# Kernel tuning notes

Hardware: AMD Instinct MI355X
Metric: run time of the kernel (lower is better)

The kernel has to match this reference:

```python
import jax, jax.numpy as jnp
import numpy as np

N_NODES = 100000
N_EDGES = 1600000
D = 128
H = 128


def setup_inputs() -> dict:
    key = jax.random.key(0)
    ks = jax.random.split(key, 8)
    x = jax.random.normal(ks[0], (N_NODES, D), dtype=jnp.float32)
    edge_index = jax.random.randint(ks[1], (2, N_EDGES), 0, N_NODES, dtype=jnp.int64)
    s = 1.0 / np.sqrt(D)
    Wl1 = jax.random.normal(ks[2], (H, D), dtype=jnp.float32) * s
    Wr1 = jax.random.normal(ks[3], (H, D), dtype=jnp.float32) * s
    b1 = jnp.zeros((H,), dtype=jnp.float32)
    sh = 1.0 / np.sqrt(H)
    Wl2 = jax.random.normal(ks[4], (H, H), dtype=jnp.float32) * sh
    Wr2 = jax.random.normal(ks[5], (H, H), dtype=jnp.float32) * sh
    b2 = jnp.zeros((H,), dtype=jnp.float32)
    return {"x": x, "edge_index": edge_index, "Wl1": Wl1, "Wr1": Wr1, "b1": b1,
            "Wl2": Wl2, "Wr2": Wr2, "b2": b2}


def reference(x, edge_index, Wl1, Wr1, b1, Wl2, Wr2, b2):
    N = x.shape[0]
    src, dst = edge_index[0], edge_index[1]
    # in-degree counts (shared across both layers)
    cnt = jax.ops.segment_sum(jnp.ones(src.shape, x.dtype), dst, num_segments=N)
    inv_cnt = (1.0 / jnp.maximum(cnt, 1.0))[:, None]  # [N,1], empty nbr -> 0 mean

    def sage(h, Wl, Wr, b):
        # mean aggregation of source features at destination nodes
        agg = jax.ops.segment_sum(h[src], dst, num_segments=N) * inv_cnt  # [N,F]
        return agg @ Wl.T + h @ Wr.T + b

    h = jax.nn.relu(sage(x, Wl1, Wr1, b1))
    return sage(h, Wl2, Wr2, b2)
```

## Files before the change

### kernel.cpp

```cpp
#include <hip/hip_runtime.h>
#include <hip/hip_bf16.h>

#define NN 100000
#define NE 1600000
#define BNODES 196
#define NB 511
#define NBLKA 256
#define CHUNK 6250

typedef unsigned short u16;
typedef unsigned int u32;
typedef unsigned char u8;
using frag  = __attribute__((ext_vector_type(8))) short;
using f32x4 = __attribute__((ext_vector_type(4))) float;
using v2f   = __attribute__((ext_vector_type(2))) float;

#define OFF_CNT   (0)
#define OFF_OFFS  (512u << 10)
#define OFF_BB    (1u << 20)
#define OFF_BSUM  ((1u << 20) + 4096)
#define OFF_H     (1310720u)
#define OFF_CSR   (2u << 20)
#define OFF_WT1   (8704u << 10)
#define OFF_WT2   ((8704u << 10) + 65536u)
#define OFF_HB    (9437184u)
#define OFF_H8    (35037184u)
#define OFF_REC   (47837184u)

__device__ __forceinline__ u16 f2bf(float f) {
    u32 u = __float_as_uint(f);
    u32 r = u + 0x7fffu + ((u >> 16) & 1u);
    return (u16)(r >> 16);
}

__device__ __forceinline__ bool edges_are_i64(const void* edges) {
    const long long* e = (const long long*)edges;
    bool ok = true;
#pragma unroll
    for (int i = 0; i < 4; i++) {
        long long v = e[i];
        if (v < 0 || v >= NN) ok = false;
    }
    return ok;
}

__device__ __forceinline__ u32 pk_fp8x4(float f0, float f1, float f2, float f3) {
    int r = __builtin_amdgcn_cvt_pk_fp8_f32(f0, f1, 0, false);
    r = __builtin_amdgcn_cvt_pk_fp8_f32(f2, f3, r, true);
    return (u32)r;
}

__global__ __launch_bounds__(256) void hist_kernel(const void* edges, int* H,
                                                   const float* x, u16* xb, u8* x8,
                                                   const float* Wl1, const float* Wr1,
                                                   const float* Wl2, const float* Wr2,
                                                   u16* Wst1, u16* Wst2) {
    __shared__ int h[512];
    int tid = threadIdx.x, blk = blockIdx.x;
    for (int i = tid; i < 512; i += 256) h[i] = 0;
    __syncthreads();

    {
        int gid = blk * 256 + tid;
        int idx = gid & 32767;
        const float* Wl = (gid < 32768) ? Wl1 : Wl2;
        const float* Wr = (gid < 32768) ? Wr1 : Wr2;
        u16* Wst = (gid < 32768) ? Wst1 : Wst2;
        int kb = idx >> 10, col = (idx >> 3) & 127, i = idx & 7;
        int k = kb * 8 + i;
        float v = (k < 128) ? Wl[col * 128 + k] : Wr[col * 128 + (k - 128)];
        Wst[idx] = f2bf(v);
    }
    {
        int u0 = blk * 6250;
        for (int u = u0 + tid; u < u0 + 6250; u += 256) {
            size_t base = (size_t)u * 8;
            float4 v0 = *(const float4*)(x + base);
            float4 v1 = *(const float4*)(x + base + 4);
            uint4 w;
            w.x = (u32)f2bf(v0.x) | ((u32)f2bf(v0.y) << 16);
            w.y = (u32)f2bf(v0.z) | ((u32)f2bf(v0.w) << 16);
            w.z = (u32)f2bf(v1.x) | ((u32)f2bf(v1.y) << 16);
            w.w = (u32)f2bf(v1.z) | ((u32)f2bf(v1.w) << 16);
            *(uint4*)(xb + base) = w;
            uint2 q;
            q.x = pk_fp8x4(v0.x, v0.y, v0.z, v0.w);
            q.y = pk_fp8x4(v1.x, v1.y, v1.z, v1.w);
            *(uint2*)(x8 + base) = q;
        }
    }
    bool f = edges_are_i64(edges);
    int lo = blk * CHUNK, hi = lo + CHUNK;
    if (f) {
        const long long* dst = (const long long*)edges + NE;
        for (int i = lo + tid; i < hi; i += 256)
            atomicAdd(&h[(int)__builtin_nontemporal_load(&dst[i]) / BNODES], 1);
    } else {
        const int* dst = (const int*)edges + NE;
        for (int i = lo + tid; i < hi; i += 256)
            atomicAdd(&h[__builtin_nontemporal_load(&dst[i]) / BNODES], 1);
    }
    __syncthreads();
    for (int i = tid; i < 512; i += 256) H[blk * 512 + i] = h[i];
}

__global__ __launch_bounds__(256) void scan1_kernel(int* H, int* bsum) {
    int tid = threadIdx.x;
    int lane = tid & 63;
    int b = blockIdx.x * 4 + (tid >> 6);
    int v0 = H[(lane * 4 + 0) * 512 + b];
    int v1 = H[(lane * 4 + 1) * 512 + b];
    int v2 = H[(lane * 4 + 2) * 512 + b];
    int v3 = H[(lane * 4 + 3) * 512 + b];
    int t = v0 + v1 + v2 + v3;
    int sc = t;
#pragma unroll
    for (int off = 1; off < 64; off <<= 1) {
        int v = __shfl_up(sc, off, 64);
        if (lane >= off) sc += v;
    }
    int excl = sc - t;
    H[(lane * 4 + 0) * 512 + b] = excl;
    H[(lane * 4 + 1) * 512 + b] = excl + v0;
    H[(lane * 4 + 2) * 512 + b] = excl + v0 + v1;
    H[(lane * 4 + 3) * 512 + b] = excl + v0 + v1 + v2;
    if (lane == 63) bsum[b] = sc;
}

__global__ void bb2_kernel(const int* bsum, int* bb) {
    __shared__ int sc[512];
    int b = threadIdx.x;
    int s = bsum[b];
    sc[b] = s;
    __syncthreads();
    for (int off = 1; off < 512; off <<= 1) {
        int v = (b >= off) ? sc[b - off] : 0;
        __syncthreads();
        sc[b] += v;
        __syncthreads();
    }
    bb[b] = sc[b] - s;
    if (b == 511) bb[512] = sc[511];
}

__global__ __launch_bounds__(256) void scatter_kernel(const void* edges, const int* H,
                                                      const int* bb, u32* rec) {
    __shared__ int cur[512];
    int tid = threadIdx.x, blk = blockIdx.x;
    for (int i = tid; i < 512; i += 256) cur[i] = bb[i] + H[blk * 512 + i];
    __syncthreads();
    bool f = edges_are_i64(edges);
    int lo = blk * CHUNK, hi = lo + CHUNK;
    if (f) {
        const long long* e = (const long long*)edges;
        for (int i = lo + tid; i < hi; i += 256) {
            int d = (int)__builtin_nontemporal_load(&e[NE + i]);
            int s = (int)__builtin_nontemporal_load(&e[i]);
            int b = d / BNODES;
            int p = atomicAdd(&cur[b], 1);
            rec[p] = ((u32)(d - b * BNODES) << 17) | (u32)s;
        }
    } else {
        const int* e = (const int*)edges;
        for (int i = lo + tid; i < hi; i += 256) {
            int d = __builtin_nontemporal_load(&e[NE + i]);
            int s = __builtin_nontemporal_load(&e[i]);
            int b = d / BNODES;
            int p = atomicAdd(&cur[b], 1);
            rec[p] = ((u32)(d - b * BNODES) << 17) | (u32)s;
        }
    }
}

__global__ __launch_bounds__(256) void bucket_csr_kernel(const u32* rec, const int* bb,
                                                         int* cnt, int* offsets, int* csr) {
    __shared__ int hcnt[200], hpre[200], hcur[200];
    int b = blockIdx.x, tid = threadIdx.x;
    int base = bb[b], total = bb[b + 1] - base;
    if (b == NB - 1 && tid < 8) csr[NE + tid] = 0;
    for (int i = tid; i < BNODES; i += 256) hcnt[i] = 0;
    __syncthreads();
    for (int i = tid; i < total; i += 256)
        atomicAdd(&hcnt[__builtin_nontemporal_load(&rec[base + i]) >> 17], 1);
    __syncthreads();
    if (tid < 64) {
        int l = tid;
        int s0 = 0, s1 = 0, s2 = 0, s3 = 0;
        if (l < 49) {
            s0 = hcnt[l * 4]; s1 = hcnt[l * 4 + 1]; s2 = hcnt[l * 4 + 2]; s3 = hcnt[l * 4 + 3];
        }
        int t0 = s0, t1 = t0 + s1, t2 = t1 + s2, t3 = t2 + s3;
        int sc = t3;
#pragma unroll
        for (int off = 1; off < 64; off <<= 1) {
            int v = __shfl_up(sc, off, 64);
            if (l >= off) sc += v;
        }
        int lbase = sc - t3;
        if (l < 49) {
            hpre[l * 4] = lbase;      hpre[l * 4 + 1] = lbase + t0;
            hpre[l * 4 + 2] = lbase + t1; hpre[l * 4 + 3] = lbase + t2;
        }
    }
    __syncthreads();
    int node0 = b * BNODES;
    for (int i = tid; i < BNODES; i += 256) {
        int n = node0 + i;
        if (n < NN) { cnt[n] = hcnt[i]; offsets[n] = base + hpre[i]; }
    }
    for (int i = tid; i < BNODES; i += 256) hcur[i] = hpre[i];
    __syncthreads();
    for (int i = tid; i < total; i += 256) {
        u32 r = __builtin_nontemporal_load(&rec[base + i]);
        int p = atomicAdd(&hcur[r >> 17], 1);
        csr[base + p] = (int)(r & 0x1FFFFu);
    }
}

__global__ __launch_bounds__(512) void fused_kernel(const u16* __restrict__ feat,
                                                    const u8* __restrict__ feat8,
                                                    const int* __restrict__ csr,
                                                    const int* __restrict__ offsets,
                                                    const int* __restrict__ cnt,
                                                    const u16* __restrict__ Wst,
                                                    const float* __restrict__ bias,
                                                    float* outF, u16* outH, u8* outH8,
                                                    int relu) {
    __shared__ __align__(16) u16 As[128][136];
    __shared__ u16 Ws[8192];
    __shared__ int sbin[128];
    __shared__ int sord[128];

    int tid = threadIdx.x;
    int lane = tid & 63;
    int w = tid >> 6;
    int slot8 = lane >> 3;
    int li8 = lane & 7;
    int nb = blockIdx.x * 128;
    int l15 = lane & 15, l4 = lane >> 4;

    if (tid < 128) sbin[tid] = 0;
    __syncthreads();
    int mydeg = 0;
    if (tid < 128) {
        int node = nb + tid;
        mydeg = (node < NN) ? cnt[node] : 0;
        atomicAdd(&sbin[min(mydeg, 127)], 1);
    }
    __syncthreads();
    if (tid < 64) {
        int s0 = sbin[2 * tid], s1 = sbin[2 * tid + 1];
        int t = s0 + s1;
        int sc = t;
#pragma unroll
        for (int off = 1; off < 64; off <<= 1) {
            int v = __shfl_up(sc, off, 64);
            if (tid >= off) sc += v;
        }
        int excl = sc - t;
        sbin[2 * tid] = excl;
        sbin[2 * tid + 1] = excl + s0;
    }
    __syncthreads();
    if (tid < 128) {
        int pos = atomicAdd(&sbin[min(mydeg, 127)], 1);
        sord[pos] = tid;
    }
    __syncthreads();

    for (int idx = tid; idx < 1024; idx += 512)
        *(float4*)&Ws[idx * 8] = *(const float4*)(Wst + idx * 8);

    for (int it = 0; it < 2; it++) {
        int nl = sord[it * 64 + w * 8 + slot8];
        int node = nb + nl;
        bool valid = node < NN;
        int beg = valid ? offsets[node] : 0;
        int deg = valid ? cnt[node] : 0;
        int md = deg;
        md = max(md, __shfl_xor(md, 8, 64));
        md = max(md, __shfl_xor(md, 16, 64));
        md = max(md, __shfl_xor(md, 32, 64));

        float acc[16];
#pragma unroll
        for (int q = 0; q < 16; q++) acc[q] = 0.f;

        if (md > 0) {
            int sCur[4];
#pragma unroll
            for (int k = 0; k < 4; k++) sCur[k] = __builtin_nontemporal_load(&csr[beg + k]);
            for (int j = 0; j < md; j += 4) {
                uint4 v[4];
#pragma unroll
                for (int k = 0; k < 4; k++)
                    v[k] = *(const uint4*)(feat8 + (size_t)sCur[k] * 128 + li8 * 16);
                int sNxt[4];
                if (j + 4 < md) {
#pragma unroll
                    for (int k = 0; k < 4; k++)
                        sNxt[k] = __builtin_nontemporal_load(&csr[beg + j + 4 + k]);
                }
#pragma unroll
                for (int k = 0; k < 4; k++) {
                    float m = (j + k < deg) ? 1.0f : 0.0f;
                    u32 wd[4] = {v[k].x, v[k].y, v[k].z, v[k].w};
#pragma unroll
                    for (int t = 0; t < 4; t++) {
                        v2f plo = __builtin_amdgcn_cvt_pk_f32_fp8((int)wd[t], false);
                        v2f phi = __builtin_amdgcn_cvt_pk_f32_fp8((int)wd[t], true);
                        acc[4 * t + 0] = fmaf(m, plo[0], acc[4 * t + 0]);
                        acc[4 * t + 1] = fmaf(m, plo[1], acc[4 * t + 1]);
                        acc[4 * t + 2] = fmaf(m, phi[0], acc[4 * t + 2]);
                        acc[4 * t + 3] = fmaf(m, phi[1], acc[4 * t + 3]);
                    }
                }
#pragma unroll
                for (int k = 0; k < 4; k++) sCur[k] = sNxt[k];
            }
        }
        float inv = (deg > 0) ? 1.0f / (float)deg : 0.0f;
        uint4 o0, o1;
        o0.x = (u32)f2bf(acc[0] * inv)  | ((u32)f2bf(acc[1] * inv) << 16);
        o0.y = (u32)f2bf(acc[2] * inv)  | ((u32)f2bf(acc[3] * inv) << 16);
        o0.z = (u32)f2bf(acc[4] * inv)  | ((u32)f2bf(acc[5] * inv) << 16);
        o0.w = (u32)f2bf(acc[6] * inv)  | ((u32)f2bf(acc[7] * inv) << 16);
        o1.x = (u32)f2bf(acc[8] * inv)  | ((u32)f2bf(acc[9] * inv) << 16);
        o1.y = (u32)f2bf(acc[10] * inv) | ((u32)f2bf(acc[11] * inv) << 16);
        o1.z = (u32)f2bf(acc[12] * inv) | ((u32)f2bf(acc[13] * inv) << 16);
        o1.w = (u32)f2bf(acc[14] * inv) | ((u32)f2bf(acc[15] * inv) << 16);
        *(uint4*)&As[nl][li8 * 16] = o0;
        *(uint4*)&As[nl][li8 * 16 + 8] = o1;
    }

    int wr = w >> 2, wc = w & 3;
    f32x4 acc2[4][2];
#pragma unroll
    for (int i = 0; i < 4; i++)
#pragma unroll
        for (int j = 0; j < 2; j++) acc2[i][j] = (f32x4){0.f, 0.f, 0.f, 0.f};

#pragma unroll
    for (int c = 0; c < 2; c++) {
#pragma unroll
        for (int h = 0; h < 2; h++) {
            __syncthreads();
            if (!(c == 0 && h == 0)) {
                for (int idx = tid; idx < 1024; idx += 512)
                    *(float4*)&Ws[idx * 8] = *(const float4*)(Wst + c * 16384 + h * 8192 + idx * 8);
            }
            if (c == 1 && h == 0) {
                for (int idx = tid; idx < 128 * 16; idx += 512) {
                    int row = idx >> 4, cc = idx & 15;
                    float4 v = make_float4(0.f, 0.f, 0.f, 0.f);
                    if (nb + row < NN)
                        v = *(const float4*)(feat + (size_t)(nb + row) * 128 + cc * 8);
                    *(float4*)&As[row][cc * 8] = v;
                }
            }
            __syncthreads();
#pragma unroll
            for (int kk2 = 0; kk2 < 2; kk2++) {
                int kk = h * 2 + kk2;
                frag a[4], bfr[2];
#pragma unroll
                for (int i = 0; i < 4; i++)
                    a[i] = *(const frag*)&As[wr * 64 + i * 16 + l15][kk * 32 + l4 * 8];
#pragma unroll
                for (int j = 0; j < 2; j++)
                    bfr[j] = *(const frag*)&Ws[((kk2 * 4 + l4) * 128 + wc * 32 + j * 16 + l15) * 8];
#pragma unroll
                for (int i = 0; i < 4; i++)
#pragma unroll
                    for (int j = 0; j < 2; j++)
                        acc2[i][j] = __builtin_amdgcn_mfma_f32_16x16x32_bf16(a[i], bfr[j], acc2[i][j], 0, 0, 0);
            }
        }
    }

    __syncthreads();

    if (relu) {
#pragma unroll
        for (int j = 0; j < 2; j++) {
            int col = wc * 32 + j * 16 + l15;
            float bv = bias[col];
#pragma unroll
            for (int i = 0; i < 4; i++) {
#pragma unroll
                for (int r = 0; r < 4; r++) {
                    float v = fmaxf(acc2[i][j][r] + bv, 0.f);
                    As[wr * 64 + i * 16 + l4 * 4 + r][col] = f2bf(v);
                }
            }
        }
        __syncthreads();
        for (int idx = tid; idx < 128 * 16; idx += 512) {
            int row = idx >> 4, cc = idx & 15;
            int node = nb + row;
            if (node < NN)
                *(uint4*)(outH + (size_t)node * 128 + cc * 8) = *(const uint4*)&As[row][cc * 8];
        }
        for (int idx = tid; idx < 128 * 8; idx += 512) {
            int row = idx >> 3, seg = idx & 7;
            int node = nb + row;
            if (node >= NN) continue;
            uint4 q0 = *(const uint4*)&As[row][seg * 16];
            uint4 q1 = *(const uint4*)&As[row][seg * 16 + 8];
            uint4 o;
            o.x = pk_fp8x4(__uint_as_float(q0.x << 16), __uint_as_float(q0.x & 0xffff0000u),
                           __uint_as_float(q0.y << 16), __uint_as_float(q0.y & 0xffff0000u));
            o.y = pk_fp8x4(__uint_as_float(q0.z << 16), __uint_as_float(q0.z & 0xffff0000u),
                           __uint_as_float(q0.w << 16), __uint_as_float(q0.w & 0xffff0000u));
            o.z = pk_fp8x4(__uint_as_float(q1.x << 16), __uint_as_float(q1.x & 0xffff0000u),
                           __uint_as_float(q1.y << 16), __uint_as_float(q1.y & 0xffff0000u));
            o.w = pk_fp8x4(__uint_as_float(q1.z << 16), __uint_as_float(q1.z & 0xffff0000u),
                           __uint_as_float(q1.w << 16), __uint_as_float(q1.w & 0xffff0000u));
            *(uint4*)(outH8 + (size_t)node * 128 + seg * 16) = o;
        }
    } else {
        float* Fs = (float*)&As[0][0];
#pragma unroll
        for (int p = 0; p < 2; p++) {
            if (p) __syncthreads();
            if (wr == p) {
#pragma unroll
                for (int j = 0; j < 2; j++) {
                    int col = wc * 32 + j * 16 + l15;
                    float bv = bias[col];
#pragma unroll
                    for (int i = 0; i < 4; i++) {
#pragma unroll
                        for (int r = 0; r < 4; r++)
                            Fs[(i * 16 + l4 * 4 + r) * 132 + col] = acc2[i][j][r] + bv;
                    }
                }
            }
            __syncthreads();
            for (int idx = tid; idx < 64 * 32; idx += 512) {
                int row = idx >> 5, cc = idx & 31;
                int node = nb + p * 64 + row;
                if (node < NN) {
                    f32x4 v = *(const f32x4*)&Fs[row * 132 + cc * 4];
                    __builtin_nontemporal_store(v, (f32x4*)(outF + (size_t)node * 128 + cc * 4));
                }
            }
        }
    }
}

extern "C" void kernel_launch(void* const* d_in, const int* in_sizes, int n_in,
                              void* d_out, int out_size, void* d_ws, size_t ws_size,
                              hipStream_t stream) {
    const float* x    = (const float*)d_in[0];
    const void* edges = d_in[1];
    const float* Wl1  = (const float*)d_in[2];
    const float* Wr1  = (const float*)d_in[3];
    const float* b1   = (const float*)d_in[4];
    const float* Wl2  = (const float*)d_in[5];
    const float* Wr2  = (const float*)d_in[6];
    const float* b2   = (const float*)d_in[7];
    float* out = (float*)d_out;

    char* ws = (char*)d_ws;
    int* cnt     = (int*)(ws + OFF_CNT);
    int* offsets = (int*)(ws + OFF_OFFS);
    int* bb      = (int*)(ws + OFF_BB);
    int* bsum    = (int*)(ws + OFF_BSUM);
    int* H       = (int*)(ws + OFF_H);
    int* csr     = (int*)(ws + OFF_CSR);
    u16* Wst1    = (u16*)(ws + OFF_WT1);
    u16* Wst2    = (u16*)(ws + OFF_WT2);
    u16* hb      = (u16*)(ws + OFF_HB);
    u8*  h8      = (u8*)(ws + OFF_H8);
    u32* rec     = (u32*)(ws + OFF_REC);

    u16* xb = (u16*)d_out;
    u8*  x8 = (u8*)d_out + 25600000;

    hist_kernel<<<NBLKA, 256, 0, stream>>>(edges, H, x, xb, x8, Wl1, Wr1, Wl2, Wr2, Wst1, Wst2);
    scan1_kernel<<<128, 256, 0, stream>>>(H, bsum);
    bb2_kernel<<<1, 512, 0, stream>>>(bsum, bb);
    scatter_kernel<<<NBLKA, 256, 0, stream>>>(edges, H, bb, rec);
    bucket_csr_kernel<<<NB, 256, 0, stream>>>(rec, bb, cnt, offsets, csr);

    int fgrid = (NN + 127) / 128;

    fused_kernel<<<fgrid, 512, 0, stream>>>(xb, x8, csr, offsets, cnt, Wst1, b1,
                                            nullptr, hb, h8, 1);
    fused_kernel<<<fgrid, 512, 0, stream>>>(hb, h8, csr, offsets, cnt, Wst2, b2,
                                            out, nullptr, nullptr, 0);
}
```

Baseline: 182.2 us.

## Schedule heaviest node tiles first and double histogram/scatter block count

Adds a single-block kernel that ranks the 782 node tiles by total in-edge count and writes a permutation. Both fused layers then read their tile index from it, so the heaviest tiles start first and tail imbalance shrinks. The histogram/scatter preprocessing also doubles its block count and halves the chunk size, and the scan is adjusted to handle 8 entries per lane. The cost is an extra serial O(n^2) ranking launch and a relocated histogram buffer.

```diff
diff --git a/kernel.cpp b/kernel.cpp
--- a/kernel.cpp
+++ b/kernel.cpp
@@ -5,8 +5,9 @@
 #define NE 1600000
 #define BNODES 196
 #define NB 511
-#define NBLKA 256
-#define CHUNK 6250
+#define NBLKA 512
+#define CHUNK 3125
+#define NTILE 782
 
 typedef unsigned short u16;
 typedef unsigned int u32;
@@ -19,13 +20,14 @@
 #define OFF_OFFS  (512u << 10)
 #define OFF_BB    (1u << 20)
 #define OFF_BSUM  ((1u << 20) + 4096)
-#define OFF_H     (1310720u)
+#define OFF_PERM  ((1u << 20) + 8192)
 #define OFF_CSR   (2u << 20)
 #define OFF_WT1   (8704u << 10)
 #define OFF_WT2   ((8704u << 10) + 65536u)
 #define OFF_HB    (9437184u)
 #define OFF_H8    (35037184u)
 #define OFF_REC   (47837184u)
+#define OFF_H     (54237184u)
 
 __device__ __forceinline__ u16 f2bf(float f) {
     u32 u = __float_as_uint(f);
@@ -62,18 +64,20 @@
 
     {
         int gid = blk * 256 + tid;
-        int idx = gid & 32767;
-        const float* Wl = (gid < 32768) ? Wl1 : Wl2;
-        const float* Wr = (gid < 32768) ? Wr1 : Wr2;
-        u16* Wst = (gid < 32768) ? Wst1 : Wst2;
-        int kb = idx >> 10, col = (idx >> 3) & 127, i = idx & 7;
-        int k = kb * 8 + i;
-        float v = (k < 128) ? Wl[col * 128 + k] : Wr[col * 128 + (k - 128)];
-        Wst[idx] = f2bf(v);
+        if (gid < 65536) {
+            int idx = gid & 32767;
+            const float* Wl = (gid < 32768) ? Wl1 : Wl2;
+            const float* Wr = (gid < 32768) ? Wr1 : Wr2;
+            u16* Wst = (gid < 32768) ? Wst1 : Wst2;
+            int kb = idx >> 10, col = (idx >> 3) & 127, i = idx & 7;
+            int k = kb * 8 + i;
+            float v = (k < 128) ? Wl[col * 128 + k] : Wr[col * 128 + (k - 128)];
+            Wst[idx] = f2bf(v);
+        }
     }
     {
-        int u0 = blk * 6250;
-        for (int u = u0 + tid; u < u0 + 6250; u += 256) {
+        int u0 = blk * 3125;
+        for (int u = u0 + tid; u < u0 + 3125; u += 256) {
             size_t base = (size_t)u * 8;
             float4 v0 = *(const float4*)(x + base);
             float4 v1 = *(const float4*)(x + base + 4);
@@ -108,22 +112,25 @@
     int tid = threadIdx.x;
     int lane = tid & 63;
     int b = blockIdx.x * 4 + (tid >> 6);
-    int v0 = H[(lane * 4 + 0) * 512 + b];
-    int v1 = H[(lane * 4 + 1) * 512 + b];
-    int v2 = H[(lane * 4 + 2) * 512 + b];
-    int v3 = H[(lane * 4 + 3) * 512 + b];
-    int t = v0 + v1 + v2 + v3;
+    int v[8];
+    int t = 0;
+#pragma unroll
+    for (int k = 0; k < 8; k++) {
+        v[k] = H[(lane * 8 + k) * 512 + b];
+        t += v[k];
+    }
     int sc = t;
 #pragma unroll
     for (int off = 1; off < 64; off <<= 1) {
-        int v = __shfl_up(sc, off, 64);
-        if (lane >= off) sc += v;
-    }
-    int excl = sc - t;
-    H[(lane * 4 + 0) * 512 + b] = excl;
-    H[(lane * 4 + 1) * 512 + b] = excl + v0;
-    H[(lane * 4 + 2) * 512 + b] = excl + v0 + v1;
-    H[(lane * 4 + 3) * 512 + b] = excl + v0 + v1 + v2;
+        int u = __shfl_up(sc, off, 64);
+        if (lane >= off) sc += u;
+    }
+    int running = sc - t;
+#pragma unroll
+    for (int k = 0; k < 8; k++) {
+        H[(lane * 8 + k) * 512 + b] = running;
+        running += v[k];
+    }
     if (lane == 63) bsum[b] = sc;
 }
 
@@ -217,11 +224,33 @@
     }
 }
 
+__global__ __launch_bounds__(1024) void perm_kernel(const int* offsets, int* perm) {
+    __shared__ int wts[NTILE];
+    int t = threadIdx.x;
+    if (t < NTILE) {
+        int n0 = t * 128;
+        int n1 = n0 + 128;
+        int s = offsets[n0];
+        int e = (n1 < NN) ? offsets[n1] : NE;
+        wts[t] = e - s;
+    }
+    __syncthreads();
+    if (t < NTILE) {
+        int w = wts[t], r = 0;
+        for (int j = 0; j < NTILE; j++) {
+            int wj = wts[j];
+            if (wj > w || (wj == w && j < t)) r++;
+        }
+        perm[r] = t;
+    }
+}
+
 __global__ __launch_bounds__(512) void fused_kernel(const u16* __restrict__ feat,
                                                     const u8* __restrict__ feat8,
                                                     const int* __restrict__ csr,
                                                     const int* __restrict__ offsets,
                                                     const int* __restrict__ cnt,
+                                                    const int* __restrict__ perm,
                                                     const u16* __restrict__ Wst,
                                                     const float* __restrict__ bias,
                                                     float* outF, u16* outH, u8* outH8,
@@ -236,7 +265,7 @@
     int w = tid >> 6;
     int slot8 = lane >> 3;
     int li8 = lane & 7;
-    int nb = blockIdx.x * 128;
+    int nb = perm[blockIdx.x] * 128;
     int l15 = lane & 15, l4 = lane >> 4;
 
     if (tid < 128) sbin[tid] = 0;
@@ -467,6 +496,7 @@
     int* offsets = (int*)(ws + OFF_OFFS);
     int* bb      = (int*)(ws + OFF_BB);
     int* bsum    = (int*)(ws + OFF_BSUM);
+    int* perm    = (int*)(ws + OFF_PERM);
     int* H       = (int*)(ws + OFF_H);
     int* csr     = (int*)(ws + OFF_CSR);
     u16* Wst1    = (u16*)(ws + OFF_WT1);
@@ -483,11 +513,10 @@
     bb2_kernel<<<1, 512, 0, stream>>>(bsum, bb);
     scatter_kernel<<<NBLKA, 256, 0, stream>>>(edges, H, bb, rec);
     bucket_csr_kernel<<<NB, 256, 0, stream>>>(rec, bb, cnt, offsets, csr);
-
-    int fgrid = (NN + 127) / 128;
-
-    fused_kernel<<<fgrid, 512, 0, stream>>>(xb, x8, csr, offsets, cnt, Wst1, b1,
+    perm_kernel<<<1, 1024, 0, stream>>>(offsets, perm);
+
+    fused_kernel<<<NTILE, 512, 0, stream>>>(xb, x8, csr, offsets, cnt, perm, Wst1, b1,
                                             nullptr, hb, h8, 1);
-    fused_kernel<<<fgrid, 512, 0, stream>>>(hb, h8, csr, offsets, cnt, Wst2, b2,
+    fused_kernel<<<NTILE, 512, 0, stream>>>(hb, h8, csr, offsets, cnt, perm, Wst2, b2,
                                             out, nullptr, nullptr, 0);
 }
```

Measured after the change: 221.7 us. 21.7% more time.
